# Optimization experiments

Measured on AMD Instinct MI355X. Metric: run time of the kernel, lower is better.

## Reference

```python
import jax, jax.numpy as jnp
from jax import lax
import numpy as np

VOCAB, EMB, H, T, B = 2500, 64, 64, 512, 256


def _gru_dir(x, mask, Wi, Wh, b, reverse):
    """Keras GRU (reset_after=True) over [B,T,D] with boolean mask [B,T].
    Masked steps carry state unchanged (Keras masking semantics; GRU output==state)."""
    bi, bh = b[0], b[1]
    if reverse:
        x = jnp.flip(x, 1)
        mask = jnp.flip(mask, 1)
    xp = x @ Wi + bi  # [B,T,3H], precompute input projections once

    def step(h, inp):
        xp_t, m_t = inp
        rec = h @ Wh + bh
        xz, xr, xh = jnp.split(xp_t, 3, axis=-1)
        rz, rr, rh = jnp.split(rec, 3, axis=-1)
        z = jax.nn.sigmoid(xz + rz)
        r = jax.nn.sigmoid(xr + rr)
        hh = jnp.tanh(xh + r * rh)
        h_new = z * h + (1.0 - z) * hh
        h = jnp.where(m_t, h_new, h)
        return h, h

    h0 = jnp.zeros((x.shape[0], Wh.shape[0]), x.dtype)
    hT, ys = lax.scan(step, h0, (jnp.swapaxes(xp, 0, 1), jnp.swapaxes(mask, 0, 1)[..., None]))
    ys = jnp.swapaxes(ys, 0, 1)  # [B,T,H]
    if reverse:
        ys = jnp.flip(ys, 1)
    return ys, hT


def _bigru_seq(x, mask, Wif, Whf, bf, Wib, Whb, bb):
    yf, _ = _gru_dir(x, mask, Wif, Whf, bf, False)
    yb, _ = _gru_dir(x, mask, Wib, Whb, bb, True)
    return jnp.concatenate([yf, yb], axis=-1)  # [B,T,2H]


def setup_inputs() -> dict:
    key = jax.random.key(0)
    ks = iter(jax.random.split(key, 40))
    s = 0.05
    d = {"tokens": jax.random.randint(next(ks), (B, T), 0, VOCAB)}
    d["emb"] = jax.random.normal(next(ks), (VOCAB, EMB), jnp.float32) * s
    for l, din in ((1, EMB), (2, 2 * H), (3, 2 * H)):
        for dr in ("f", "b"):
            d[f"wi{l}{dr}"] = jax.random.normal(next(ks), (din, 3 * H), jnp.float32) * s
            d[f"wh{l}{dr}"] = jax.random.normal(next(ks), (H, 3 * H), jnp.float32) * s
            d[f"bb{l}{dr}"] = jax.random.normal(next(ks), (2, 3 * H), jnp.float32) * s
    d["wd1"] = jax.random.normal(next(ks), (2 * H, 64), jnp.float32) * s
    d["bd1"] = jnp.zeros((64,), jnp.float32)
    d["wd2"] = jax.random.normal(next(ks), (64, 64), jnp.float32) * s
    d["bd2"] = jnp.zeros((64,), jnp.float32)
    d["wd3"] = jax.random.normal(next(ks), (64, 64), jnp.float32) * s
    d["bd3"] = jnp.zeros((64,), jnp.float32)
    d["wo"] = jax.random.normal(next(ks), (64, 28), jnp.float32) * s
    d["bo"] = jnp.zeros((28,), jnp.float32)
    return d


def reference(tokens, emb, wi1f, wh1f, bb1f, wi1b, wh1b, bb1b,
              wi2f, wh2f, bb2f, wi2b, wh2b, bb2b,
              wi3f, wh3f, bb3f, wi3b, wh3b, bb3b,
              wd1, bd1, wd2, bd2, wd3, bd3, wo, bo):
    mask = tokens > 0  # mask_zero=True
    x = emb[tokens]  # [B,T,EMB]
    x = _bigru_seq(x, mask, wi1f, wh1f, bb1f, wi1b, wh1b, bb1b)
    x = _bigru_seq(x, mask, wi2f, wh2f, bb2f, wi2b, wh2b, bb2b)
    _, hf = _gru_dir(x, mask, wi3f, wh3f, bb3f, False)
    _, hb = _gru_dir(x, mask, wi3b, wh3b, bb3b, True)
    x = jnp.concatenate([hf, hb], axis=-1)  # [B,2H]
    x = jax.nn.relu(x @ wd1 + bd1)
    x = jax.nn.relu(x @ wd2 + bd2)
    x = jax.nn.relu(x @ wd3 + bd3)
    return jax.nn.sigmoid(x @ wo + bo)  # [B,28]
```

## Files before the change

kernel.cpp:

```cpp
#include <hip/hip_runtime.h>
#include <hip/hip_bf16.h>
#include <cstddef>

#define T_SEQ 512
#define BATCH 256
#define RTOT (BATCH * T_SEQ)

__device__ __forceinline__ float fsigmoid(float x) {
    return 1.0f / (1.0f + __expf(-x));
}
__device__ __forceinline__ float ftanh(float x) {
    return 1.0f - 2.0f / (__expf(2.0f * x) + 1.0f);
}

template <int DIN, bool EMBED>
__global__ __launch_bounds__(192) void proj_kernel(
    const float* __restrict__ X, const int* __restrict__ tokens,
    const float* __restrict__ emb,
    const float* __restrict__ Wf, const float* __restrict__ bf_,
    const float* __restrict__ Wb, const float* __restrict__ bb_,
    float* __restrict__ xpf, float* __restrict__ xpb)
{
    constexpr int ROWS = 32;
    constexpr int PAD = 36;
    __shared__ __align__(16) float xt[DIN][PAD];
    const int r0 = blockIdx.x * ROWS;
    const int tid = threadIdx.x;

    for (int e = tid; e < ROWS * DIN; e += 192) {
        const int row = e / DIN;
        const int i = e % DIN;
        float v;
        if (EMBED) {
            v = emb[(size_t)tokens[r0 + row] * 64 + i];
        } else {
            v = X[(size_t)(r0 + row) * DIN + i];
        }
        xt[i][row] = v;
    }
    __syncthreads();

    const int col = tid;
    #pragma unroll
    for (int d = 0; d < 2; d++) {
        const float* __restrict__ W = d ? Wb : Wf;
        const float* __restrict__ bi = d ? bb_ : bf_;
        float* __restrict__ outp = d ? xpb : xpf;
        float acc[ROWS];
        const float b0 = bi[col];
        #pragma unroll
        for (int r = 0; r < ROWS; r++) acc[r] = b0;
        #pragma unroll 4
        for (int i = 0; i < DIN; i++) {
            const float w = W[i * 192 + col];
            #pragma unroll
            for (int r = 0; r < ROWS; r += 4) {
                const float4 x4 = *(const float4*)&xt[i][r];
                acc[r + 0] = fmaf(x4.x, w, acc[r + 0]);
                acc[r + 1] = fmaf(x4.y, w, acc[r + 1]);
                acc[r + 2] = fmaf(x4.z, w, acc[r + 2]);
                acc[r + 3] = fmaf(x4.w, w, acc[r + 3]);
            }
        }
        #pragma unroll
        for (int r = 0; r < ROWS; r++) {
            outp[(size_t)(r0 + r) * 192 + col] = acc[r];
        }
    }
}

__global__ __launch_bounds__(192) void gru_scan(
    const float* __restrict__ xpf, const float* __restrict__ xpb,
    const float* __restrict__ whf, const float* __restrict__ whb,
    const float* __restrict__ bbf, const float* __restrict__ bbb,
    const int* __restrict__ tokens,
    float* __restrict__ y,
    float* __restrict__ hfinal)
{
    const int chain = blockIdx.x;
    const int b = chain >> 1;
    const int dir = chain & 1;
    const float* __restrict__ xp = dir ? xpb : xpf;
    const float* __restrict__ wh = dir ? whb : whf;
    const float* __restrict__ bb = dir ? bbb : bbf;
    const int k = threadIdx.x;

    float whk[64];
    #pragma unroll
    for (int i = 0; i < 64; i++) whk[i] = wh[i * 192 + k];
    const float bhk = bb[192 + k];

    __shared__ __align__(16) float h_lds[64];
    __shared__ float z_lds[64];
    __shared__ float r_lds[64];
    if (k < 64) h_lds[k] = 0.0f;
    __syncthreads();

    const int t0 = dir ? (T_SEQ - 1) : 0;
    const int st = dir ? -1 : 1;
    const size_t base = (size_t)b * T_SEQ;

    float xv = xp[(base + t0) * 192 + k];
    int tok = tokens[base + t0];

    for (int t = 0; t < T_SEQ; t++) {
        const int tn = (t + 1 < T_SEQ) ? (t + 1) : t;
        const int te_n = t0 + st * tn;
        const float xv_n = xp[(base + te_n) * 192 + k];
        const int tok_n = tokens[base + te_n];

        float acc = bhk;
        #pragma unroll
        for (int i = 0; i < 64; i += 4) {
            const float4 h4 = *(const float4*)&h_lds[i];
            acc = fmaf(h4.x, whk[i + 0], acc);
            acc = fmaf(h4.y, whk[i + 1], acc);
            acc = fmaf(h4.z, whk[i + 2], acc);
            acc = fmaf(h4.w, whk[i + 3], acc);
        }
        if (k < 64) {
            z_lds[k] = fsigmoid(xv + acc);
        } else if (k < 128) {
            r_lds[k - 64] = fsigmoid(xv + acc);
        }
        __syncthreads();
        if (k >= 128) {
            const int j = k - 128;
            const float r = r_lds[j];
            const float hh = ftanh(xv + r * acc);
            const float z = z_lds[j];
            const float hold = h_lds[j];
            float hnew = z * hold + (1.0f - z) * hh;
            if (!(tok > 0)) hnew = hold;
            h_lds[j] = hnew;
            if (y) {
                const int te = t0 + st * t;
                y[(base + te) * 128 + (dir << 6) + j] = hnew;
            }
        }
        __syncthreads();
        xv = xv_n;
        tok = tok_n;
    }
    if (hfinal && k >= 128) {
        hfinal[b * 128 + (dir << 6) + (k - 128)] = h_lds[k - 128];
    }
}

__global__ __launch_bounds__(64) void mlp_kernel(
    const float* __restrict__ hcat,
    const float* __restrict__ wd1, const float* __restrict__ bd1,
    const float* __restrict__ wd2, const float* __restrict__ bd2,
    const float* __restrict__ wd3, const float* __restrict__ bd3,
    const float* __restrict__ wo, const float* __restrict__ bo,
    float* __restrict__ outp)
{
    const int b = blockIdx.x;
    const int j = threadIdx.x;
    __shared__ float x0[128];
    __shared__ float x1[64];
    x0[j] = hcat[b * 128 + j];
    x0[j + 64] = hcat[b * 128 + 64 + j];
    __syncthreads();
    float a = bd1[j];
    #pragma unroll 4
    for (int i = 0; i < 128; i++) a = fmaf(x0[i], wd1[i * 64 + j], a);
    a = fmaxf(a, 0.0f);
    x1[j] = a;
    __syncthreads();
    float a2 = bd2[j];
    #pragma unroll 4
    for (int i = 0; i < 64; i++) a2 = fmaf(x1[i], wd2[i * 64 + j], a2);
    a2 = fmaxf(a2, 0.0f);
    __syncthreads();
    x1[j] = a2;
    __syncthreads();
    float a3 = bd3[j];
    #pragma unroll 4
    for (int i = 0; i < 64; i++) a3 = fmaf(x1[i], wd3[i * 64 + j], a3);
    a3 = fmaxf(a3, 0.0f);
    __syncthreads();
    x1[j] = a3;
    __syncthreads();
    if (j < 28) {
        float o = bo[j];
        #pragma unroll 4
        for (int i = 0; i < 64; i++) o = fmaf(x1[i], wo[i * 28 + j], o);
        outp[b * 28 + j] = fsigmoid(o);
    }
}

extern "C" void kernel_launch(void* const* d_in, const int* in_sizes, int n_in,
                              void* d_out, int out_size, void* d_ws, size_t ws_size,
                              hipStream_t stream)
{
    const int* tokens  = (const int*)d_in[0];
    const float* emb   = (const float*)d_in[1];
    const float* wi1f  = (const float*)d_in[2];
    const float* wh1f  = (const float*)d_in[3];
    const float* bb1f  = (const float*)d_in[4];
    const float* wi1b  = (const float*)d_in[5];
    const float* wh1b  = (const float*)d_in[6];
    const float* bb1b  = (const float*)d_in[7];
    const float* wi2f  = (const float*)d_in[8];
    const float* wh2f  = (const float*)d_in[9];
    const float* bb2f  = (const float*)d_in[10];
    const float* wi2b  = (const float*)d_in[11];
    const float* wh2b  = (const float*)d_in[12];
    const float* bb2b  = (const float*)d_in[13];
    const float* wi3f  = (const float*)d_in[14];
    const float* wh3f  = (const float*)d_in[15];
    const float* bb3f  = (const float*)d_in[16];
    const float* wi3b  = (const float*)d_in[17];
    const float* wh3b  = (const float*)d_in[18];
    const float* bb3b  = (const float*)d_in[19];
    const float* wd1   = (const float*)d_in[20];
    const float* bd1   = (const float*)d_in[21];
    const float* wd2   = (const float*)d_in[22];
    const float* bd2   = (const float*)d_in[23];
    const float* wd3   = (const float*)d_in[24];
    const float* bd3   = (const float*)d_in[25];
    const float* wo    = (const float*)d_in[26];
    const float* bo    = (const float*)d_in[27];

    float* y    = (float*)d_ws;
    float* xpf  = y + (size_t)RTOT * 128;
    float* xpb  = xpf + (size_t)RTOT * 192;
    float* hcat = y;

    const dim3 pb(192), pg(RTOT / 32);

    proj_kernel<64, true><<<pg, pb, 0, stream>>>(nullptr, tokens, emb,
                                                 wi1f, bb1f, wi1b, bb1b, xpf, xpb);
    gru_scan<<<512, 192, 0, stream>>>(xpf, xpb, wh1f, wh1b, bb1f, bb1b,
                                      tokens, y, nullptr);
    proj_kernel<128, false><<<pg, pb, 0, stream>>>(y, nullptr, nullptr,
                                                   wi2f, bb2f, wi2b, bb2b, xpf, xpb);
    gru_scan<<<512, 192, 0, stream>>>(xpf, xpb, wh2f, wh2b, bb2f, bb2b,
                                      tokens, y, nullptr);
    proj_kernel<128, false><<<pg, pb, 0, stream>>>(y, nullptr, nullptr,
                                                   wi3f, bb3f, wi3b, bb3b, xpf, xpb);
    gru_scan<<<512, 192, 0, stream>>>(xpf, xpb, wh3f, wh3b, bb3f, bb3b,
                                      tokens, nullptr, hcat);
    mlp_kernel<<<256, 64, 0, stream>>>(hcat, wd1, bd1, wd2, bd2, wd3, bd3,
                                       wo, bo, (float*)d_out);
}
```

Baseline: 1.549 ms.

## Cut GRU scan to one barrier per step with redundant per-wave hidden update

Each of the three 64-thread waves now recomputes the candidate and hidden-state update for all 64 units. The shared gate buffer and the hidden-state buffer are double-buffered, so each timestep needs only one __syncthreads instead of two. The previous hidden value is kept in a register, inputs are prefetched two steps ahead, and the recurrent dot product uses four independent accumulators to shorten the FMA dependency chain. In exchange, the tanh and blend work is done three times, and correctness relies on each wave rewriting the full hidden vector with identical values from every wave.

```diff
diff --git a/kernel.cpp b/kernel.cpp
--- a/kernel.cpp
+++ b/kernel.cpp
@@ -69,7 +69,7 @@
     }
 }
 
-__global__ __launch_bounds__(192) void gru_scan(
+__global__ __launch_bounds__(192, 1) void gru_scan(
     const float* __restrict__ xpf, const float* __restrict__ xpb,
     const float* __restrict__ whf, const float* __restrict__ whb,
     const float* __restrict__ bbf, const float* __restrict__ bbb,
@@ -84,66 +84,80 @@
     const float* __restrict__ wh = dir ? whb : whf;
     const float* __restrict__ bb = dir ? bbb : bbf;
     const int k = threadIdx.x;
+    const int j = k & 63;
+    const int g = k >> 6;
 
     float whk[64];
     #pragma unroll
     for (int i = 0; i < 64; i++) whk[i] = wh[i * 192 + k];
     const float bhk = bb[192 + k];
 
-    __shared__ __align__(16) float h_lds[64];
-    __shared__ float z_lds[64];
-    __shared__ float r_lds[64];
-    if (k < 64) h_lds[k] = 0.0f;
+    __shared__ __align__(16) float h_lds[2][64];
+    __shared__ __align__(16) float4 gates[2][64];
+
+    if (k < 64) h_lds[0][k] = 0.0f;
     __syncthreads();
 
     const int t0 = dir ? (T_SEQ - 1) : 0;
     const int st = dir ? -1 : 1;
     const size_t base = (size_t)b * T_SEQ;
 
-    float xv = xp[(base + t0) * 192 + k];
-    int tok = tokens[base + t0];
+    float xv0 = xp[(base + t0) * 192 + k];
+    int tk0 = tokens[base + t0];
+    float xv1 = xp[(base + t0 + st) * 192 + k];
+    int tk1 = tokens[base + t0 + st];
+
+    float hprev = 0.0f;
+    int p = 0;
 
     for (int t = 0; t < T_SEQ; t++) {
-        const int tn = (t + 1 < T_SEQ) ? (t + 1) : t;
+        const int tn = (t + 2 < T_SEQ) ? (t + 2) : (T_SEQ - 1);
         const int te_n = t0 + st * tn;
-        const float xv_n = xp[(base + te_n) * 192 + k];
-        const int tok_n = tokens[base + te_n];
-
-        float acc = bhk;
+        const float xv2 = xp[(base + te_n) * 192 + k];
+        const int tk2 = tokens[base + te_n];
+
+        float hreg[64];
+        #pragma unroll
+        for (int i = 0; i < 64; i += 4)
+            *(float4*)&hreg[i] = *(const float4*)&h_lds[p][i];
+
+        float a0 = bhk, a1 = 0.0f, a2 = 0.0f, a3 = 0.0f;
         #pragma unroll
         for (int i = 0; i < 64; i += 4) {
-            const float4 h4 = *(const float4*)&h_lds[i];
-            acc = fmaf(h4.x, whk[i + 0], acc);
-            acc = fmaf(h4.y, whk[i + 1], acc);
-            acc = fmaf(h4.z, whk[i + 2], acc);
-            acc = fmaf(h4.w, whk[i + 3], acc);
-        }
-        if (k < 64) {
-            z_lds[k] = fsigmoid(xv + acc);
-        } else if (k < 128) {
-            r_lds[k - 64] = fsigmoid(xv + acc);
+            a0 = fmaf(hreg[i + 0], whk[i + 0], a0);
+            a1 = fmaf(hreg[i + 1], whk[i + 1], a1);
+            a2 = fmaf(hreg[i + 2], whk[i + 2], a2);
+            a3 = fmaf(hreg[i + 3], whk[i + 3], a3);
+        }
+        const float acc = (a0 + a1) + (a2 + a3);
+
+        if (g == 0) {
+            gates[p][j].x = fsigmoid(xv0 + acc);
+        } else if (g == 1) {
+            gates[p][j].y = fsigmoid(xv0 + acc);
+        } else {
+            gates[p][j].z = acc;
+            gates[p][j].w = xv0;
         }
         __syncthreads();
-        if (k >= 128) {
-            const int j = k - 128;
-            const float r = r_lds[j];
-            const float hh = ftanh(xv + r * acc);
-            const float z = z_lds[j];
-            const float hold = h_lds[j];
-            float hnew = z * hold + (1.0f - z) * hh;
-            if (!(tok > 0)) hnew = hold;
-            h_lds[j] = hnew;
-            if (y) {
-                const int te = t0 + st * t;
-                y[(base + te) * 128 + (dir << 6) + j] = hnew;
-            }
-        }
-        __syncthreads();
-        xv = xv_n;
-        tok = tok_n;
-    }
-    if (hfinal && k >= 128) {
-        hfinal[b * 128 + (dir << 6) + (k - 128)] = h_lds[k - 128];
+
+        const float4 gt = gates[p][j];
+        const float hh = ftanh(gt.w + gt.y * gt.z);
+        const float z = gt.x;
+        float hnew = z * hprev + (1.0f - z) * hh;
+        if (!(tk0 > 0)) hnew = hprev;
+        h_lds[p ^ 1][j] = hnew;
+        if (g == 2 && y) {
+            const int te = t0 + st * t;
+            y[(base + te) * 128 + (dir << 6) + j] = hnew;
+        }
+        hprev = hnew;
+        p ^= 1;
+        xv0 = xv1; xv1 = xv2;
+        tk0 = tk1; tk1 = tk2;
+    }
+    if (hfinal && g == 2) {
+        hfinal[b * 128 + (dir << 6) + j] = hprev;
     }
 }
 
```

New measurement: 1.647 ms. 1.06x slower.

## Run each GRU chain in one wavefront with readlane broadcast of hidden state

Applied to the files above, without the earlier changes.

The recurrent scan now runs one 64-lane wavefront per chain. Each lane owns one hidden unit and holds all three gate weight columns (192 registers). The hidden state is broadcast with readlane instead of passing through LDS, which removes both block-wide barriers per timestep. Input projections are prefetched two steps ahead. In exchange each lane does three times the FMAs serially and carries heavy register pressure, with a risk of spills. Only 512 waves occupy the GPU.

```diff
diff --git a/kernel.cpp b/kernel.cpp
--- a/kernel.cpp
+++ b/kernel.cpp
@@ -69,7 +69,7 @@
     }
 }
 
-__global__ __launch_bounds__(192) void gru_scan(
+__global__ __launch_bounds__(64, 1) void gru_scan(
     const float* __restrict__ xpf, const float* __restrict__ xpb,
     const float* __restrict__ whf, const float* __restrict__ whb,
     const float* __restrict__ bbf, const float* __restrict__ bbb,
@@ -83,67 +83,72 @@
     const float* __restrict__ xp = dir ? xpb : xpf;
     const float* __restrict__ wh = dir ? whb : whf;
     const float* __restrict__ bb = dir ? bbb : bbf;
-    const int k = threadIdx.x;
-
-    float whk[64];
+    const int j = threadIdx.x;
+
+    float wz[64], wr[64], wc[64];
     #pragma unroll
-    for (int i = 0; i < 64; i++) whk[i] = wh[i * 192 + k];
-    const float bhk = bb[192 + k];
-
-    __shared__ __align__(16) float h_lds[64];
-    __shared__ float z_lds[64];
-    __shared__ float r_lds[64];
-    if (k < 64) h_lds[k] = 0.0f;
-    __syncthreads();
+    for (int i = 0; i < 64; i++) {
+        wz[i] = wh[i * 192 + j];
+        wr[i] = wh[i * 192 + 64 + j];
+        wc[i] = wh[i * 192 + 128 + j];
+    }
+    const float bz = bb[192 + j];
+    const float br = bb[192 + 64 + j];
+    const float bh = bb[192 + 128 + j];
 
     const int t0 = dir ? (T_SEQ - 1) : 0;
     const int st = dir ? -1 : 1;
     const size_t base = (size_t)b * T_SEQ;
 
-    float xv = xp[(base + t0) * 192 + k];
-    int tok = tokens[base + t0];
+    float xz0, xr0, xh0, xz1, xr1, xh1;
+    int tk0, tk1;
+    {
+        const float* p = xp + (base + t0) * 192 + j;
+        xz0 = p[0]; xr0 = p[64]; xh0 = p[128];
+        tk0 = tokens[base + t0];
+    }
+    {
+        const float* p = xp + (base + t0 + st) * 192 + j;
+        xz1 = p[0]; xr1 = p[64]; xh1 = p[128];
+        tk1 = tokens[base + t0 + st];
+    }
+
+    float h = 0.0f;
 
     for (int t = 0; t < T_SEQ; t++) {
-        const int tn = (t + 1 < T_SEQ) ? (t + 1) : t;
+        const int tn = (t + 2 < T_SEQ) ? (t + 2) : (T_SEQ - 1);
         const int te_n = t0 + st * tn;
-        const float xv_n = xp[(base + te_n) * 192 + k];
-        const int tok_n = tokens[base + te_n];
-
-        float acc = bhk;
+        const float* pn = xp + (base + te_n) * 192 + j;
+        const float xz2 = pn[0], xr2 = pn[64], xh2 = pn[128];
+        const int tk2 = tokens[base + te_n];
+
+        float az = bz, ar = br, ah = bh;
         #pragma unroll
-        for (int i = 0; i < 64; i += 4) {
-            const float4 h4 = *(const float4*)&h_lds[i];
-            acc = fmaf(h4.x, whk[i + 0], acc);
-            acc = fmaf(h4.y, whk[i + 1], acc);
-            acc = fmaf(h4.z, whk[i + 2], acc);
-            acc = fmaf(h4.w, whk[i + 3], acc);
-        }
-        if (k < 64) {
-            z_lds[k] = fsigmoid(xv + acc);
-        } else if (k < 128) {
-            r_lds[k - 64] = fsigmoid(xv + acc);
-        }
-        __syncthreads();
-        if (k >= 128) {
-            const int j = k - 128;
-            const float r = r_lds[j];
-            const float hh = ftanh(xv + r * acc);
-            const float z = z_lds[j];
-            const float hold = h_lds[j];
-            float hnew = z * hold + (1.0f - z) * hh;
-            if (!(tok > 0)) hnew = hold;
-            h_lds[j] = hnew;
-            if (y) {
-                const int te = t0 + st * t;
-                y[(base + te) * 128 + (dir << 6) + j] = hnew;
-            }
-        }
-        __syncthreads();
-        xv = xv_n;
-        tok = tok_n;
-    }
-    if (hfinal && k >= 128) {
-        hfinal[b * 128 + (dir << 6) + (k - 128)] = h_lds[k - 128];
+        for (int i = 0; i < 64; i++) {
+            const float hi = __int_as_float(
+                __builtin_amdgcn_readlane(__float_as_int(h), i));
+            az = fmaf(hi, wz[i], az);
+            ar = fmaf(hi, wr[i], ar);
+            ah = fmaf(hi, wc[i], ah);
+        }
+
+        const float z = fsigmoid(xz0 + az);
+        const float r = fsigmoid(xr0 + ar);
+        const float cand = ftanh(xh0 + r * ah);
+        float hnew = z * h + (1.0f - z) * cand;
+        if (!(tk0 > 0)) hnew = h;
+        h = hnew;
+
+        if (y) {
+            const int te = t0 + st * t;
+            y[(base + te) * 128 + (dir << 6) + j] = h;
+        }
+
+        xz0 = xz1; xr0 = xr1; xh0 = xh1; tk0 = tk1;
+        xz1 = xz2; xr1 = xr2; xh1 = xh2; tk1 = tk2;
+    }
+    if (hfinal) {
+        hfinal[b * 128 + (dir << 6) + j] = h;
     }
 }
 
@@ -232,16 +237,16 @@
 
     proj_kernel<64, true><<<pg, pb, 0, stream>>>(nullptr, tokens, emb,
                                                  wi1f, bb1f, wi1b, bb1b, xpf, xpb);
-    gru_scan<<<512, 192, 0, stream>>>(xpf, xpb, wh1f, wh1b, bb1f, bb1b,
-                                      tokens, y, nullptr);
+    gru_scan<<<512, 64, 0, stream>>>(xpf, xpb, wh1f, wh1b, bb1f, bb1b,
+                                     tokens, y, nullptr);
     proj_kernel<128, false><<<pg, pb, 0, stream>>>(y, nullptr, nullptr,
                                                    wi2f, bb2f, wi2b, bb2b, xpf, xpb);
-    gru_scan<<<512, 192, 0, stream>>>(xpf, xpb, wh2f, wh2b, bb2f, bb2b,
-                                      tokens, y, nullptr);
+    gru_scan<<<512, 64, 0, stream>>>(xpf, xpb, wh2f, wh2b, bb2f, bb2b,
+                                     tokens, y, nullptr);
     proj_kernel<128, false><<<pg, pb, 0, stream>>>(y, nullptr, nullptr,
                                                    wi3f, bb3f, wi3b, bb3b, xpf, xpb);
-    gru_scan<<<512, 192, 0, stream>>>(xpf, xpb, wh3f, wh3b, bb3f, bb3b,
-                                      tokens, nullptr, hcat);
+    gru_scan<<<512, 64, 0, stream>>>(xpf, xpb, wh3f, wh3b, bb3f, bb3b,
+                                     tokens, nullptr, hcat);
     mlp_kernel<<<256, 64, 0, stream>>>(hcat, wd1, bd1, wd2, bd2, wd3, bd3,
                                        wo, bo, (float*)d_out);
 }
```

Result: slower. 2.351 ms (+51.7%).
